# Optimization experiments

Measured on AMD Instinct MI355X. Metric: run time of the kernel, lower is better.

## Reference

```python
import jax, jax.numpy as jnp
import numpy as np

H, HD, RD = 16, 128, 64          # n_heads, head_dim, rope_dim
CD = HD - RD                      # content_dim = 64
THETA = 10000.0


def apply_rope(x, cos, sin):
    # x: [B,H,T,RD]; cos/sin: [T,RD//2] broadcast over B,H
    d = x.shape[-1] // 2
    x1, x2 = x[..., :d], x[..., d:]
    return jnp.concatenate([x1 * cos - x2 * sin, x1 * sin + x2 * cos], axis=-1)


def setup_inputs() -> dict:
    key = jax.random.key(0)
    ks = jax.random.split(key, 9)
    d_model, q_rank, d_latent = 2048, 512, 512
    B, T = 2, 2048
    s = 0.02
    return {
        "x": jax.random.normal(ks[0], (B, T, d_model), dtype=jnp.float32),
        "Wq_down": jax.random.normal(ks[1], (d_model, q_rank), dtype=jnp.float32) * s,
        "Wq_up": jax.random.normal(ks[2], (q_rank, H * CD), dtype=jnp.float32) * s,
        "Wq_rope": jax.random.normal(ks[3], (d_model, H * RD), dtype=jnp.float32) * s,
        "Wkv_down": jax.random.normal(ks[4], (d_model, d_latent), dtype=jnp.float32) * s,
        "Wk_up": jax.random.normal(ks[5], (d_latent, H * CD), dtype=jnp.float32) * s,
        "Wv_up": jax.random.normal(ks[6], (d_latent, H * HD), dtype=jnp.float32) * s,
        "Wk_rope": jax.random.normal(ks[7], (d_model, H * RD), dtype=jnp.float32) * s,
        "Wo": jax.random.normal(ks[8], (H * HD, d_model), dtype=jnp.float32) * s,
    }


def reference(x, Wq_down, Wq_up, Wq_rope, Wkv_down, Wk_up, Wv_up, Wk_rope, Wo):
    B, T, _ = x.shape

    # low-rank projections
    q_content = (x @ Wq_down) @ Wq_up            # [B,T,H*CD]
    q_pos = x @ Wq_rope                          # [B,T,H*RD]
    kv_latent = x @ Wkv_down                     # [B,T,d_latent]
    k_content = kv_latent @ Wk_up                # [B,T,H*CD]
    k_pos = x @ Wk_rope                          # [B,T,H*RD]
    v = kv_latent @ Wv_up                        # [B,T,H*HD]

    def split_heads(t, d):
        return t.reshape(B, T, H, d).transpose(0, 2, 1, 3)  # [B,H,T,d]

    q_content = split_heads(q_content, CD)
    q_pos = split_heads(q_pos, RD)
    k_content = split_heads(k_content, CD)
    k_pos = split_heads(k_pos, RD)
    v = split_heads(v, HD)

    # rotary tables: [T, RD//2]
    inv_freq = 1.0 / (THETA ** (jnp.arange(0, RD, 2, dtype=jnp.float32) / RD))
    freqs = jnp.arange(T, dtype=jnp.float32)[:, None] * inv_freq[None, :]
    cos, sin = jnp.cos(freqs), jnp.sin(freqs)

    q_pos = apply_rope(q_pos, cos, sin)
    k_pos = apply_rope(k_pos, cos, sin)

    q = jnp.concatenate([q_content, q_pos], axis=-1)  # [B,H,T,HD]
    k = jnp.concatenate([k_content, k_pos], axis=-1)  # [B,H,T,HD]

    # causal SDPA, scale = 1/sqrt(head_dim)
    scale = 1.0 / jnp.sqrt(jnp.asarray(HD, dtype=q.dtype))
    scores = jnp.einsum("bhqd,bhkd->bhqk", q, k) * scale
    causal = jnp.tril(jnp.ones((T, T), dtype=bool))
    scores = jnp.where(causal, scores, jnp.finfo(scores.dtype).min)
    attn = jax.nn.softmax(scores, axis=-1)
    out = jnp.einsum("bhqk,bhkd->bhqd", attn, v)      # [B,H,T,HD]

    out = out.transpose(0, 2, 1, 3).reshape(B, T, H * HD)
    return out @ Wo
```

## Files before the change

### kernel.cpp

```cpp
#include <hip/hip_runtime.h>
#include <hip/hip_bf16.h>
#include <stdint.h>
#include <math.h>

#define H_ 16
#define HD_ 128
#define RD_ 64
#define CD_ 64
#define DM_ 2048
#define QR_ 512
#define DL_ 512
#define B_ 2
#define T_ 2048
#define M_TOT (B_*T_)

typedef __attribute__((ext_vector_type(8))) short short8;
typedef __attribute__((ext_vector_type(4))) float f32x4;
typedef __attribute__((ext_vector_type(16))) float f32x16;

__device__ __forceinline__ unsigned short f2b_hw(float f){
  __hip_bfloat16 h = __float2bfloat16(f);
  union { __hip_bfloat16 h; unsigned short u; } c; c.h = h; return c.u;
}
__device__ __forceinline__ float b2f(unsigned short b){
  union { unsigned u; float f; } a; a.u = ((unsigned)b) << 16;
  return a.f;
}
__device__ __forceinline__ unsigned pack2(float lo, float hi){
  __hip_bfloat162 h2 = __float22bfloat162_rn(make_float2(lo, hi));
  union { __hip_bfloat162 h; unsigned u; } c; c.h = h2; return c.u;
}

#define GLOAD16(g, l) __builtin_amdgcn_global_load_lds( \
    (__attribute__((address_space(1))) void*)(g), \
    (__attribute__((address_space(3))) void*)(l), 16, 0, 0)

__global__ void cast_f32_bf16(const float* __restrict__ src,
                              unsigned short* __restrict__ dst, int n){
  int i = (blockIdx.x * blockDim.x + threadIdx.x) * 4;
  if (i < n){
    float4 v = *(const float4*)(src + i);
    ushort4 o;
    o.x = f2b_hw(v.x); o.y = f2b_hw(v.y); o.z = f2b_hw(v.z); o.w = f2b_hw(v.w);
    *(ushort4*)(dst + i) = o;
  }
}

struct TTe { const float* src; unsigned short* dst; int K, N, blk0; };
struct TT8 { TTe e[8]; };

__global__ void transpose_cast8(TT8 tab){
  __shared__ float tile[32][33];
  int bid = blockIdx.x;
  const float* src = tab.e[0].src;
  unsigned short* dst = tab.e[0].dst;
  int K = tab.e[0].K, N = tab.e[0].N, loc = bid;
  #pragma unroll
  for (int j = 1; j < 8; j++){
    if (bid >= tab.e[j].blk0){
      src = tab.e[j].src; dst = tab.e[j].dst;
      K = tab.e[j].K; N = tab.e[j].N; loc = bid - tab.e[j].blk0;
    }
  }
  int cols = N / 32;
  int n0 = (loc % cols) * 32, k0 = (loc / cols) * 32;
  int tx = threadIdx.x, ty = threadIdx.y;
  #pragma unroll
  for (int r = ty; r < 32; r += 8)
    tile[r][tx] = src[(size_t)(k0 + r) * N + n0 + tx];
  __syncthreads();
  #pragma unroll
  for (int r = ty; r < 32; r += 8)
    dst[(size_t)(n0 + r) * K + k0 + tx] = f2b_hw(tile[tx][r]);
}

template<int MODE>
__global__ __launch_bounds__(256) void gemm_bt(
    const unsigned short* __restrict__ A, int lda,
    const unsigned short* __restrict__ Bt,
    void* __restrict__ Cv, void* __restrict__ Cv2, void* __restrict__ Cv3,
    int ldc, int N, int K)
{
  __shared__ unsigned short As[128 * 32];
  __shared__ unsigned short Bs[128 * 32];
  int tid = threadIdx.x;

  int gx = gridDim.x;
  int nwg = gx * gridDim.y;
  int lin = blockIdx.x + gx * blockIdx.y;
  int q8 = nwg >> 3;
  int nl = (lin & 7) * q8 + (lin >> 3);
  int m0 = (nl / gx) * 128, n0 = (nl % gx) * 128;

  int lane = tid & 63, w = tid >> 6;
  int wr = (w >> 1) * 64, wc = (w & 1) * 64;
  int mr = lane & 15, kg = lane >> 4;

  const unsigned short* Ag = A  + (size_t)(m0 + (tid >> 2)) * lda + ((tid & 3) << 3);
  const unsigned short* Bg = Bt + (size_t)(n0 + (tid >> 2)) * K + ((tid & 3) << 3);

  f32x4 acc[4][4];
  #pragma unroll
  for (int i = 0; i < 4; i++)
    #pragma unroll
    for (int j = 0; j < 4; j++)
      acc[i][j] = (f32x4){0.f, 0.f, 0.f, 0.f};

  for (int k0 = 0; k0 < K; k0 += 32) {
    #pragma unroll
    for (int j = 0; j < 2; j++) {
      GLOAD16(Ag + (size_t)j * 64 * lda, &As[j * 2048 + tid * 8]);
      GLOAD16(Bg + (size_t)j * 64 * K, &Bs[j * 2048 + tid * 8]);
    }
    Ag += 32; Bg += 32;
    __syncthreads();
    short8 af[4], bf[4];
    #pragma unroll
    for (int i = 0; i < 4; i++)
      af[i] = *(const short8*)&As[(wr + i * 16 + mr) * 32 + kg * 8];
    #pragma unroll
    for (int j = 0; j < 4; j++)
      bf[j] = *(const short8*)&Bs[(wc + j * 16 + mr) * 32 + kg * 8];
    __builtin_amdgcn_s_setprio(1);
    #pragma unroll
    for (int i = 0; i < 4; i++)
      #pragma unroll
      for (int j = 0; j < 4; j++)
        acc[i][j] = __builtin_amdgcn_mfma_f32_16x16x32_bf16(af[i], bf[j], acc[i][j], 0, 0, 0);
    __builtin_amdgcn_s_setprio(0);
    __syncthreads();
  }

  if (MODE == 1) {
    float* C = (float*)Cv;
    #pragma unroll
    for (int i = 0; i < 4; i++)
      #pragma unroll
      for (int j = 0; j < 4; j++)
        #pragma unroll
        for (int r = 0; r < 4; r++) {
          int row = m0 + wr + i * 16 + kg * 4 + r;
          int col = n0 + wc + j * 16 + mr;
          C[(size_t)row * ldc + col] = acc[i][j][r];
        }
  } else if (MODE == 0) {
    unsigned short* C = (unsigned short*)Cv;
    #pragma unroll
    for (int i = 0; i < 4; i++)
      #pragma unroll
      for (int j = 0; j < 4; j++)
        #pragma unroll
        for (int r = 0; r < 4; r++) {
          int row = m0 + wr + i * 16 + kg * 4 + r;
          int col = n0 + wc + j * 16 + mr;
          C[(size_t)row * ldc + col] = f2b_hw(acc[i][j][r]);
        }
  } else if (MODE == 2) {
    unsigned short* qhp = (unsigned short*)Cv;
    #pragma unroll
    for (int i = 0; i < 4; i++)
      #pragma unroll
      for (int j = 0; j < 4; j++) {
        int colb = n0 + wc + j * 16 + mr;
        int h = colb >> 6, d = colb & 63;
        #pragma unroll
        for (int r = 0; r < 4; r++) {
          int gr = m0 + wr + i * 16 + kg * 4 + r;
          size_t idx = ((size_t)((gr >> 11) * H_ + h) * T_ + (gr & (T_-1))) * 128 + d;
          qhp[idx] = f2b_hw(acc[i][j][r]);
        }
      }
  } else if (MODE == 3) {
    unsigned short* khp = (unsigned short*)Cv;
    unsigned short* vtp = (unsigned short*)Cv2;
    if (n0 < 1024) {
      #pragma unroll
      for (int i = 0; i < 4; i++)
        #pragma unroll
        for (int j = 0; j < 4; j++) {
          int colb = n0 + wc + j * 16 + mr;
          int h = colb >> 6, d = colb & 63;
          #pragma unroll
          for (int r = 0; r < 4; r++) {
            int gr = m0 + wr + i * 16 + kg * 4 + r;
            size_t idx = ((size_t)((gr >> 11) * H_ + h) * T_ + (gr & (T_-1))) * 128 + d;
            khp[idx] = f2b_hw(acc[i][j][r]);
          }
        }
    } else {
      #pragma unroll
      for (int i = 0; i < 4; i++)
        #pragma unroll
        for (int j = 0; j < 4; j++) {
          int c2 = n0 + wc + j * 16 + mr - 1024;
          int h = c2 >> 7, d = c2 & 127;
          int gr0 = m0 + wr + i * 16 + kg * 4;
          int b = gr0 >> 11, t0 = gr0 & (T_-1);
          ushort4 o;
          o.x = f2b_hw(acc[i][j][0]); o.y = f2b_hw(acc[i][j][1]);
          o.z = f2b_hw(acc[i][j][2]); o.w = f2b_hw(acc[i][j][3]);
          size_t idx = ((size_t)(b * H_ + h) * 128 + d) * T_ + t0;
          *(ushort4*)&vtp[idx] = o;
        }
    }
  } else {
    if (n0 < 1024) {
      unsigned short* C = (unsigned short*)Cv;
      #pragma unroll
      for (int i = 0; i < 4; i++)
        #pragma unroll
        for (int j = 0; j < 4; j++)
          #pragma unroll
          for (int r = 0; r < 4; r++) {
            int row = m0 + wr + i * 16 + kg * 4 + r;
            int col = n0 + wc + j * 16 + mr;
            C[(size_t)row * ldc + col] = f2b_hw(acc[i][j][r]);
          }
    } else {
      const bool isq = (n0 < 2048);
      unsigned short* dst = (unsigned short*)(isq ? Cv2 : Cv3);
      int cbase = n0 - (isq ? 1024 : 2048);
      #pragma unroll
      for (int jp = 0; jp < 2; jp++) {
        int colA = wc + jp * 16 + mr;
        int cA = cbase + colA;
        int h = cA >> 6, jr = cA & 63;
        float invf = exp2f(-(float)jr * 0.4152410118750f);
        #pragma unroll
        for (int i = 0; i < 4; i++)
          #pragma unroll
          for (int r = 0; r < 4; r++) {
            int gr = m0 + wr + i * 16 + kg * 4 + r;
            int t = gr & (T_ - 1);
            float fr = (float)t * invf;
            float s_, c_;
            sincosf(fr, &s_, &c_);
            float x1 = acc[i][jp][r], x2 = acc[i][jp + 2][r];
            size_t base = ((size_t)((gr >> 11) * H_ + h) * T_ + t) * 128 + 64;
            dst[base + jr]      = f2b_hw(x1 * c_ - x2 * s_);
            dst[base + jr + 32] = f2b_hw(x1 * s_ + x2 * c_);
          }
      }
    }
  }
}

__global__ __launch_bounds__(256, 2) void attn_fwd7(
    const unsigned short* __restrict__ qh,
    const unsigned short* __restrict__ kh,
    const unsigned short* __restrict__ vt,
    unsigned short* __restrict__ ao)
{
  __shared__ __align__(16) unsigned short lds[4 * 8192];

  const int tid  = threadIdx.x;
  const int lane = tid & 63, w = tid >> 6;
  const int l31  = lane & 31, hi = lane >> 5;
  const int bh = blockIdx.y;
  const int b  = bh >> 4, hd = bh & 15;
  int qt = blockIdx.x;
  if (bh >= 16) qt = 15 - qt;
  const int q0w   = qt * 128 + w * 32;
  const int qg    = q0w + l31;
  const int qmaxw = q0w + 31;
  const int nt    = 2 * qt + 2;

  const unsigned short* Qg = qh + (size_t)bh * T_ * 128;
  const unsigned short* Kg = kh + (size_t)bh * T_ * 128;
  const unsigned short* Vg = vt + (size_t)bh * 128 * T_;

  short8 qf[8];
  #pragma unroll
  for (int kc = 0; kc < 8; kc++)
    qf[kc] = *(const short8*)&Qg[(size_t)qg * 128 + kc * 16 + hi * 8];

  f32x16 accO[4];
  #pragma unroll
  for (int sb = 0; sb < 4; sb++)
    #pragma unroll
    for (int r = 0; r < 16; r++) accO[sb][r] = 0.f;

  float m = -1e30f, lsum = 0.f;
  const float SC = 0.12751743f;

  int krow[4], kwof[4], vrow[4], vwof[4];
  #pragma unroll
  for (int jj = 0; jj < 4; jj++){
    int r_ = (w * 4 + jj) * 4 + (lane >> 4);
    krow[jj] = r_;
    kwof[jj] = r_ * 128 + ((((lane & 15) * 16) ^ ((r_ & 7) << 4)) >> 1);
    int d_ = (w * 4 + jj) * 8 + (lane >> 3);
    vrow[jj] = d_;
    vwof[jj] = d_ * 64 + ((((lane & 7) * 16) ^ ((d_ & 7) << 4)) >> 1);
  }
  const int kcol = (lane & 15) * 8;
  const int vcol = (lane & 7) * 8;

  uint4 kst[4], vst[4];

#define REG_LOAD(kvt) do {                                                    \
    int kv0s = (kvt) * 64;                                                    \
    _Pragma("unroll")                                                         \
    for (int j_ = 0; j_ < 4; j_++) {                                          \
      kst[j_] = *(const uint4*)&Kg[(size_t)(kv0s + krow[j_]) * 128 + kcol];   \
      vst[j_] = *(const uint4*)&Vg[(size_t)vrow[j_] * T_ + kv0s + vcol];      \
    }                                                                         \
  } while (0)

#define DS_WRITE(bufi) do {                                                   \
    unsigned short* ksb_ = lds + (bufi) * 8192;                               \
    unsigned short* vsb_ = lds + 16384 + (bufi) * 8192;                       \
    _Pragma("unroll")                                                         \
    for (int j_ = 0; j_ < 4; j_++) {                                          \
      *(uint4*)&ksb_[kwof[j_]] = kst[j_];                                     \
      *(uint4*)&vsb_[vwof[j_]] = vst[j_];                                     \
    }                                                                         \
  } while (0)

  REG_LOAD(0);
  DS_WRITE(0);
  if (nt > 1) REG_LOAD(1);
  asm volatile("s_waitcnt lgkmcnt(0)" ::: "memory");
  __builtin_amdgcn_s_barrier();
  __builtin_amdgcn_sched_barrier(0);

  for (int t = 0; t < nt; t++) {
    const int cur = t & 1;
    if (t + 1 < nt) DS_WRITE(cur ^ 1);
    if (t + 2 < nt) REG_LOAD(t + 2);
    const int kv0 = t * 64;
    if (kv0 <= qmaxw) {
      const unsigned short* Kb = lds + cur * 8192;
      const unsigned short* Vb = lds + 16384 + cur * 8192;

      f32x16 sa0, sa1;
      #pragma unroll
      for (int r = 0; r < 16; r++) { sa0[r] = 0.f; sa1[r] = 0.f; }
      __builtin_amdgcn_s_setprio(1);
      #pragma unroll
      for (int kc = 0; kc < 8; kc++) {
        int co = (kc * 32 + hi * 16);
        int r0 = l31;
        short8 kf0 = *(const short8*)&Kb[r0 * 128 + ((co ^ ((r0 & 7) << 4)) >> 1)];
        sa0 = __builtin_amdgcn_mfma_f32_32x32x16_bf16(kf0, qf[kc], sa0, 0, 0, 0);
        int r1 = 32 + l31;
        short8 kf1 = *(const short8*)&Kb[r1 * 128 + ((co ^ ((r1 & 7) << 4)) >> 1)];
        sa1 = __builtin_amdgcn_mfma_f32_32x32x16_bf16(kf1, qf[kc], sa1, 0, 0, 0);
      }
      __builtin_amdgcn_s_setprio(0);

      float p0[16], p1[16];
      float pmax = -1e30f;
      bool needMask = (kv0 + 63 > q0w);
      if (needMask) {
        #pragma unroll
        for (int r = 0; r < 16; r++) {
          int crow = (r & 3) + 8 * (r >> 2) + 4 * hi;
          float v0 = sa0[r] * SC;
          float v1 = sa1[r] * SC;
          if (kv0 + crow > qg)      v0 = -1e30f;
          if (kv0 + 32 + crow > qg) v1 = -1e30f;
          p0[r] = v0; p1[r] = v1;
          pmax = fmaxf(pmax, fmaxf(v0, v1));
        }
      } else {
        #pragma unroll
        for (int r = 0; r < 16; r++) {
          float v0 = sa0[r] * SC;
          float v1 = sa1[r] * SC;
          p0[r] = v0; p1[r] = v1;
          pmax = fmaxf(pmax, fmaxf(v0, v1));
        }
      }
      pmax = fmaxf(pmax, __shfl_xor(pmax, 32, 64));
      if (!__all(pmax <= m + 8.f)) {
        float mn  = fmaxf(m, pmax);
        float fac = exp2f(m - mn);
        m = mn;
        lsum *= fac;
        #pragma unroll
        for (int sb = 0; sb < 4; sb++)
          #pragma unroll
          for (int r = 0; r < 16; r++) accO[sb][r] *= fac;
      }
      float ls = 0.f;
      #pragma unroll
      for (int r = 0; r < 16; r++) {
        p0[r] = exp2f(p0[r] - m);
        p1[r] = exp2f(p1[r] - m);
        ls += p0[r] + p1[r];
      }
      ls += __shfl_xor(ls, 32, 64);
      lsum += ls;

      #pragma unroll
      for (int kc2 = 0; kc2 < 4; kc2++) {
        unsigned A01, A23, B01, B23;
        if (kc2 == 0) { A01 = pack2(p0[0], p0[1]);  A23 = pack2(p0[2], p0[3]);
                        B01 = pack2(p0[4], p0[5]);  B23 = pack2(p0[6], p0[7]); }
        else if (kc2 == 1) { A01 = pack2(p0[8], p0[9]);   A23 = pack2(p0[10], p0[11]);
                             B01 = pack2(p0[12], p0[13]); B23 = pack2(p0[14], p0[15]); }
        else if (kc2 == 2) { A01 = pack2(p1[0], p1[1]);  A23 = pack2(p1[2], p1[3]);
                             B01 = pack2(p1[4], p1[5]);  B23 = pack2(p1[6], p1[7]); }
        else { A01 = pack2(p1[8], p1[9]);   A23 = pack2(p1[10], p1[11]);
               B01 = pack2(p1[12], p1[13]); B23 = pack2(p1[14], p1[15]); }
        asm("v_permlane32_swap_b32 %0, %1" : "+v"(A01), "+v"(B01));
        asm("v_permlane32_swap_b32 %0, %1" : "+v"(A23), "+v"(B23));
        union { unsigned u[4]; short8 v; } pk;
        pk.u[0] = A01; pk.u[1] = A23; pk.u[2] = B01; pk.u[3] = B23;
        short8 pa = pk.v;
        __builtin_amdgcn_s_setprio(1);
        #pragma unroll
        for (int sb = 0; sb < 4; sb++) {
          int d = sb * 32 + l31;
          short8 vf = *(const short8*)&Vb[d * 64 + (((kc2 * 32 + hi * 16) ^ ((d & 7) << 4)) >> 1)];
          accO[sb] = __builtin_amdgcn_mfma_f32_32x32x16_bf16(vf, pa, accO[sb], 0, 0, 0);
        }
        __builtin_amdgcn_s_setprio(0);
      }
    }
    __builtin_amdgcn_sched_barrier(0);
    asm volatile("s_waitcnt lgkmcnt(0)" ::: "memory");
    __builtin_amdgcn_s_barrier();
    __builtin_amdgcn_sched_barrier(0);
  }

  float rl = 1.0f / lsum;
  size_t orow = ((size_t)b * T_ + qg) * (H_*HD_) + hd * 128;
  #pragma unroll
  for (int sb = 0; sb < 4; sb++)
    #pragma unroll
    for (int g = 0; g < 4; g++) {
      ushort4 o;
      o.x = f2b_hw(accO[sb][4 * g + 0] * rl);
      o.y = f2b_hw(accO[sb][4 * g + 1] * rl);
      o.z = f2b_hw(accO[sb][4 * g + 2] * rl);
      o.w = f2b_hw(accO[sb][4 * g + 3] * rl);
      *(ushort4*)&ao[orow + sb * 32 + 8 * g + 4 * hi] = o;
    }
#undef REG_LOAD
#undef DS_WRITE
}

extern "C" void kernel_launch(void* const* d_in, const int* in_sizes, int n_in,
                              void* d_out, int out_size, void* d_ws, size_t ws_size,
                              hipStream_t stream)
{
  (void)in_sizes; (void)n_in; (void)out_size; (void)ws_size;
  const float* x        = (const float*)d_in[0];
  const float* Wq_down  = (const float*)d_in[1];
  const float* Wq_up    = (const float*)d_in[2];
  const float* Wq_rope  = (const float*)d_in[3];
  const float* Wkv_down = (const float*)d_in[4];
  const float* Wk_up    = (const float*)d_in[5];
  const float* Wv_up    = (const float*)d_in[6];
  const float* Wk_rope  = (const float*)d_in[7];
  const float* Wo       = (const float*)d_in[8];

  char* ws = (char*)d_ws;
  unsigned short* xb      = (unsigned short*)(ws + 0);
  unsigned short* Wdall   = (unsigned short*)(ws + 16777216);
  unsigned short* WquT    = (unsigned short*)(ws + 29360128);
  unsigned short* WkcvT   = (unsigned short*)(ws + 30408704);
  unsigned short* WoT     = (unsigned short*)(ws + 33554432);
  unsigned short* projall = (unsigned short*)(ws + 41943040);
  unsigned short* qh      = (unsigned short*)(ws + 67108864);
  unsigned short* kh      = (unsigned short*)(ws + 83886080);
  unsigned short* vt      = (unsigned short*)(ws + 100663296);
  unsigned short* ao      = (unsigned short*)(ws + 117440512);

  dim3 tb(32, 8);

  cast_f32_bf16<<<(M_TOT * DM_ / 4 + 255) / 256, 256, 0, stream>>>(x, xb, M_TOT * DM_);

  TT8 tab;
  int blk = 0;
  tab.e[0] = { Wq_down,  Wdall,               DM_, QR_,     blk }; blk += (QR_/32)*(DM_/32);
  tab.e[1] = { Wkv_down, Wdall + 512*2048,    DM_, DL_,     blk }; blk += (DL_/32)*(DM_/32);
  tab.e[2] = { Wq_rope,  Wdall + 1024*2048,   DM_, H_*RD_,  blk }; blk += (H_*RD_/32)*(DM_/32);
  tab.e[3] = { Wk_rope,  Wdall + 2048*2048,   DM_, H_*RD_,  blk }; blk += (H_*RD_/32)*(DM_/32);
  tab.e[4] = { Wq_up,    WquT,                QR_, H_*CD_,  blk }; blk += (H_*CD_/32)*(QR_/32);
  tab.e[5] = { Wk_up,    WkcvT,               DL_, H_*CD_,  blk }; blk += (H_*CD_/32)*(DL_/32);
  tab.e[6] = { Wv_up,    WkcvT + 1024*512,    DL_, H_*HD_,  blk }; blk += (H_*HD_/32)*(DL_/32);
  tab.e[7] = { Wo,       WoT,                 H_*HD_, DM_,  blk }; blk += (DM_/32)*(H_*HD_/32);
  transpose_cast8<<<blk, tb, 0, stream>>>(tab);

  gemm_bt<4><<<dim3(3072/128, M_TOT/128), 256, 0, stream>>>(xb, DM_, Wdall, projall, qh, kh, 1024, 3072, DM_);
  gemm_bt<2><<<dim3(1024/128, M_TOT/128), 256, 0, stream>>>(projall, 1024, WquT, qh, nullptr, nullptr, 0, 1024, QR_);
  gemm_bt<3><<<dim3(3072/128, M_TOT/128), 256, 0, stream>>>(projall + 512, 1024, WkcvT, kh, vt, nullptr, 0, 3072, DL_);

  attn_fwd7<<<dim3(16, 32), 256, 0, stream>>>(qh, kh, vt, ao);

  gemm_bt<1><<<dim3(DM_/128, M_TOT/128), 256, 0, stream>>>(ao, 2048, WoT, d_out, nullptr, nullptr, DM_, DM_, H_*HD_);
}
```

Before: 348.8 us.

## Merge q-up and kv-up GEMMs into one launch and precompute RoPE table

Merges the q_content up-projection and the k/v up-projection GEMMs into a single launch (new MODE 5). It relies on WquT and WkcvT sitting next to each other in the workspace, and switches the A pointer by column tile so each part reads its own half of projall. A small kernel also precomputes a cos/sin table, so the rope epilogue does a table lookup instead of calling sincosf per element. The aim is to save one launch, balance the two small grids into one larger grid, and cut transcendental work in the epilogue. The table adds a small extra kernel and is written past the previous workspace end, which assumes the workspace has room for it.

```diff
diff --git a/kernel.cpp b/kernel.cpp
--- a/kernel.cpp
+++ b/kernel.cpp
@@ -46,6 +46,16 @@
   }
 }
 
+__global__ void rope_table(float2* __restrict__ tab){
+  int idx = blockIdx.x * 256 + threadIdx.x;
+  int t = idx >> 5, j = idx & 31;
+  float invf = exp2f(-(float)j * 0.4152410118750f);
+  float fr = (float)t * invf;
+  float s, c;
+  sincosf(fr, &s, &c);
+  tab[idx] = make_float2(c, s);
+}
+
 struct TTe { const float* src; unsigned short* dst; int K, N, blk0; };
 struct TT8 { TTe e[8]; };
 
@@ -79,6 +89,7 @@
     const unsigned short* __restrict__ A, int lda,
     const unsigned short* __restrict__ Bt,
     void* __restrict__ Cv, void* __restrict__ Cv2, void* __restrict__ Cv3,
+    const float2* __restrict__ tab,
     int ldc, int N, int K)
 {
   __shared__ unsigned short As[128 * 32];
@@ -96,8 +107,11 @@
   int wr = (w >> 1) * 64, wc = (w & 1) * 64;
   int mr = lane & 15, kg = lane >> 4;
 
-  const unsigned short* Ag = A  + (size_t)(m0 + (tid >> 2)) * lda + ((tid & 3) << 3);
-  const unsigned short* Bg = Bt + (size_t)(n0 + (tid >> 2)) * K + ((tid & 3) << 3);
+  const unsigned short* Aeff = A;
+  if (MODE == 5 && n0 >= 1024) Aeff = A + 512;
+
+  const unsigned short* Ag = Aeff + (size_t)(m0 + (tid >> 2)) * lda + ((tid & 3) << 3);
+  const unsigned short* Bg = Bt   + (size_t)(n0 + (tid >> 2)) * K + ((tid & 3) << 3);
 
   f32x4 acc[4][4];
   #pragma unroll
@@ -143,67 +157,7 @@
           int col = n0 + wc + j * 16 + mr;
           C[(size_t)row * ldc + col] = acc[i][j][r];
         }
-  } else if (MODE == 0) {
-    unsigned short* C = (unsigned short*)Cv;
-    #pragma unroll
-    for (int i = 0; i < 4; i++)
-      #pragma unroll
-      for (int j = 0; j < 4; j++)
-        #pragma unroll
-        for (int r = 0; r < 4; r++) {
-          int row = m0 + wr + i * 16 + kg * 4 + r;
-          int col = n0 + wc + j * 16 + mr;
-          C[(size_t)row * ldc + col] = f2b_hw(acc[i][j][r]);
-        }
-  } else if (MODE == 2) {
-    unsigned short* qhp = (unsigned short*)Cv;
-    #pragma unroll
-    for (int i = 0; i < 4; i++)
-      #pragma unroll
-      for (int j = 0; j < 4; j++) {
-        int colb = n0 + wc + j * 16 + mr;
-        int h = colb >> 6, d = colb & 63;
-        #pragma unroll
-        for (int r = 0; r < 4; r++) {
-          int gr = m0 + wr + i * 16 + kg * 4 + r;
-          size_t idx = ((size_t)((gr >> 11) * H_ + h) * T_ + (gr & (T_-1))) * 128 + d;
-          qhp[idx] = f2b_hw(acc[i][j][r]);
-        }
-      }
-  } else if (MODE == 3) {
-    unsigned short* khp = (unsigned short*)Cv;
-    unsigned short* vtp = (unsigned short*)Cv2;
-    if (n0 < 1024) {
-      #pragma unroll
-      for (int i = 0; i < 4; i++)
-        #pragma unroll
-        for (int j = 0; j < 4; j++) {
-          int colb = n0 + wc + j * 16 + mr;
-          int h = colb >> 6, d = colb & 63;
-          #pragma unroll
-          for (int r = 0; r < 4; r++) {
-            int gr = m0 + wr + i * 16 + kg * 4 + r;
-            size_t idx = ((size_t)((gr >> 11) * H_ + h) * T_ + (gr & (T_-1))) * 128 + d;
-            khp[idx] = f2b_hw(acc[i][j][r]);
-          }
-        }
-    } else {
-      #pragma unroll
-      for (int i = 0; i < 4; i++)
-        #pragma unroll
-        for (int j = 0; j < 4; j++) {
-          int c2 = n0 + wc + j * 16 + mr - 1024;
-          int h = c2 >> 7, d = c2 & 127;
-          int gr0 = m0 + wr + i * 16 + kg * 4;
-          int b = gr0 >> 11, t0 = gr0 & (T_-1);
-          ushort4 o;
-          o.x = f2b_hw(acc[i][j][0]); o.y = f2b_hw(acc[i][j][1]);
-          o.z = f2b_hw(acc[i][j][2]); o.w = f2b_hw(acc[i][j][3]);
-          size_t idx = ((size_t)(b * H_ + h) * 128 + d) * T_ + t0;
-          *(ushort4*)&vtp[idx] = o;
-        }
-    }
-  } else {
+  } else if (MODE == 4) {
     if (n0 < 1024) {
       unsigned short* C = (unsigned short*)Cv;
       #pragma unroll
@@ -225,22 +179,53 @@
         int colA = wc + jp * 16 + mr;
         int cA = cbase + colA;
         int h = cA >> 6, jr = cA & 63;
-        float invf = exp2f(-(float)jr * 0.4152410118750f);
         #pragma unroll
         for (int i = 0; i < 4; i++)
           #pragma unroll
           for (int r = 0; r < 4; r++) {
             int gr = m0 + wr + i * 16 + kg * 4 + r;
             int t = gr & (T_ - 1);
-            float fr = (float)t * invf;
-            float s_, c_;
-            sincosf(fr, &s_, &c_);
+            float2 cs = tab[t * 32 + jr];
             float x1 = acc[i][jp][r], x2 = acc[i][jp + 2][r];
             size_t base = ((size_t)((gr >> 11) * H_ + h) * T_ + t) * 128 + 64;
-            dst[base + jr]      = f2b_hw(x1 * c_ - x2 * s_);
-            dst[base + jr + 32] = f2b_hw(x1 * s_ + x2 * c_);
+            dst[base + jr]      = f2b_hw(x1 * cs.x - x2 * cs.y);
+            dst[base + jr + 32] = f2b_hw(x1 * cs.y + x2 * cs.x);
           }
       }
+    }
+  } else {
+    if (n0 < 2048) {
+      unsigned short* dstp = (unsigned short*)(n0 < 1024 ? Cv : Cv2);
+      int cb = (n0 < 1024) ? n0 : n0 - 1024;
+      #pragma unroll
+      for (int i = 0; i < 4; i++)
+        #pragma unroll
+        for (int j = 0; j < 4; j++) {
+          int colb = cb + wc + j * 16 + mr;
+          int h = colb >> 6, d = colb & 63;
+          #pragma unroll
+          for (int r = 0; r < 4; r++) {
+            int gr = m0 + wr + i * 16 + kg * 4 + r;
+            size_t idx = ((size_t)((gr >> 11) * H_ + h) * T_ + (gr & (T_-1))) * 128 + d;
+            dstp[idx] = f2b_hw(acc[i][j][r]);
+          }
+        }
+    } else {
+      unsigned short* vtp = (unsigned short*)Cv3;
+      #pragma unroll
+      for (int i = 0; i < 4; i++)
+        #pragma unroll
+        for (int j = 0; j < 4; j++) {
+          int c2 = n0 + wc + j * 16 + mr - 2048;
+          int h = c2 >> 7, d = c2 & 127;
+          int gr0 = m0 + wr + i * 16 + kg * 4;
+          int b = gr0 >> 11, t0 = gr0 & (T_-1);
+          ushort4 o;
+          o.x = f2b_hw(acc[i][j][0]); o.y = f2b_hw(acc[i][j][1]);
+          o.z = f2b_hw(acc[i][j][2]); o.w = f2b_hw(acc[i][j][3]);
+          size_t idx = ((size_t)(b * H_ + h) * 128 + d) * T_ + t0;
+          *(ushort4*)&vtp[idx] = o;
+        }
     }
   }
 }
@@ -468,10 +453,12 @@
   unsigned short* kh      = (unsigned short*)(ws + 83886080);
   unsigned short* vt      = (unsigned short*)(ws + 100663296);
   unsigned short* ao      = (unsigned short*)(ws + 117440512);
+  float2*         ctab    = (float2*)(ws + 134217728);
 
   dim3 tb(32, 8);
 
   cast_f32_bf16<<<(M_TOT * DM_ / 4 + 255) / 256, 256, 0, stream>>>(x, xb, M_TOT * DM_);
+  rope_table<<<256, 256, 0, stream>>>(ctab);
 
   TT8 tab;
   int blk = 0;
@@ -485,11 +472,13 @@
   tab.e[7] = { Wo,       WoT,                 H_*HD_, DM_,  blk }; blk += (DM_/32)*(H_*HD_/32);
   transpose_cast8<<<blk, tb, 0, stream>>>(tab);
 
-  gemm_bt<4><<<dim3(3072/128, M_TOT/128), 256, 0, stream>>>(xb, DM_, Wdall, projall, qh, kh, 1024, 3072, DM_);
-  gemm_bt<2><<<dim3(1024/128, M_TOT/128), 256, 0, stream>>>(projall, 1024, WquT, qh, nullptr, nullptr, 0, 1024, QR_);
-  gemm_bt<3><<<dim3(3072/128, M_TOT/128), 256, 0, stream>>>(projall + 512, 1024, WkcvT, kh, vt, nullptr, 0, 3072, DL_);
+  gemm_bt<4><<<dim3(3072/128, M_TOT/128), 256, 0, stream>>>(
+      xb, DM_, Wdall, projall, qh, kh, ctab, 1024, 3072, DM_);
+  gemm_bt<5><<<dim3(4096/128, M_TOT/128), 256, 0, stream>>>(
+      projall, 1024, WquT, qh, kh, vt, nullptr, 0, 4096, DL_);
 
   attn_fwd7<<<dim3(16, 32), 256, 0, stream>>>(qh, kh, vt, ao);
 
-  gemm_bt<1><<<dim3(DM_/128, M_TOT/128), 256, 0, stream>>>(ao, 2048, WoT, d_out, nullptr, nullptr, DM_, DM_, H_*HD_);
-}
+  gemm_bt<1><<<dim3(DM_/128, M_TOT/128), 256, 0, stream>>>(
+      ao, 2048, WoT, d_out, nullptr, nullptr, nullptr, DM_, DM_, H_*HD_);
+}
```

Measured after the change: 345.1 us. Within noise of the previous version (-1.1%).
